# Performance work log

Measured on AMD Instinct MI355X. Metric: run time of the kernel, lower is better.

## Reference

```python
import jax, jax.numpy as jnp
import numpy as np

B, S, H, E, K = 4, 4096, 4096, 64, 2
AUX_W = 0.01


def setup_inputs() -> dict:
    key = jax.random.key(0)
    k1, k2 = jax.random.split(key)
    hidden_states = jax.random.normal(k1, (B, S, H), dtype=jnp.float32)
    W = jax.random.normal(k2, (E, H), dtype=jnp.float32) * 0.02  # router weight [num_experts, hidden_size]
    return {"hidden_states": hidden_states, "W": W}


def reference(hidden_states, W):
    b, s, h = hidden_states.shape
    n = b * s  # tokens
    e, k = W.shape[0], K
    # router logits: [b, s, e] -> [n, e]
    logits = jnp.einsum('bsh,eh->bse', hidden_states, W).reshape(n, e)
    probs = jax.nn.softmax(logits, axis=-1)
    # top-k routing
    routing_weights, selected_experts = jax.lax.top_k(probs, k)  # [n, k]
    routing_weights = routing_weights / jnp.sum(routing_weights, axis=-1, keepdims=True)
    # scatter_add normalized weights back onto expert axis: [n, e]
    rows = jnp.arange(n)[:, None]
    router_prob_per_expert = jnp.zeros((n, e), dtype=probs.dtype).at[rows, selected_experts].add(routing_weights)
    aux_loss = jnp.mean(jnp.sum(router_prob_per_expert, axis=0) * jnp.mean(router_prob_per_expert, axis=0)) * e * AUX_W
    # expert mask via one-hot: [n, k, e]
    dispatch_mask = jax.nn.one_hot(selected_experts, e, dtype=hidden_states.dtype)
    combine_weights = routing_weights.reshape(b, s, k, 1)
    return (dispatch_mask, combine_weights, aux_loss)
```

## Files before the change

kernel.cpp:

```cpp
#include <hip/hip_runtime.h>
#include <cstdint>

#define N_TOK 16384
#define HID   4096
#define NEXP  64
#define AUXW  0.01f
#define TOKB  32
#define KC    64
#define NCH   (HID/KC)
#define IMG_CHUNK 24576

typedef __attribute__((ext_vector_type(4))) _Float16 f16x4;
typedef __attribute__((ext_vector_type(8))) _Float16 f16x8;
typedef __attribute__((ext_vector_type(4))) float f32x4;

typedef const __attribute__((address_space(1))) void gvoid_t;
typedef __attribute__((address_space(3))) void lvoid_t;

__device__ __forceinline__ void async_cp16(const void* g, void* l) {
  __builtin_amdgcn_global_load_lds((gvoid_t*)g, (lvoid_t*)l, 16, 0, 0);
}

__device__ __forceinline__ void split3_f4(float4 p, f16x4& H, f16x4& M, f16x4& L) {
  float f[4] = {p.x, p.y, p.z, p.w};
#pragma unroll
  for (int j = 0; j < 4; ++j) {
    _Float16 h = (_Float16)f[j];
    float r1 = f[j] - (float)h;
    _Float16 m = (_Float16)r1;
    float r2 = r1 - (float)m;
    H[j] = h; M[j] = m; L[j] = (_Float16)r2;
  }
}

__global__ void presplit_w(const float* __restrict__ Wg, char* __restrict__ img) {
  int id = blockIdx.x * 256 + threadIdx.x;
  int row = id >> 9;
  int rem = id & 511;
  int chunk = rem >> 3;
  int g = rem & 7;
  const float* src = Wg + (size_t)row * HID + chunk * KC + g * 8;
  float4 p0 = *(const float4*)src;
  float4 p1 = *(const float4*)(src + 4);
  f16x4 h0, m0, l0, h1, m1, l1;
  split3_f4(p0, h0, m0, l0);
  split3_f4(p1, h1, m1, l1);
  char* base = img + (size_t)chunk * IMG_CHUNK + row * 128 + ((g ^ (row & 7)) << 4);
  *(f16x4*)(base)         = h0;  *(f16x4*)(base + 8)     = h1;
  *(f16x4*)(base + 8192)  = m0;  *(f16x4*)(base + 8200)  = m1;
  *(f16x4*)(base + 16384) = l0;  *(f16x4*)(base + 16392) = l1;
}

__global__ __launch_bounds__(256, 2) void router_main(
    const float* __restrict__ hs, const char* __restrict__ wimg,
    float* __restrict__ out, float* __restrict__ Sacc) {
  __shared__ __align__(16) char smem[61440];
  char* Abuf = smem;
  char* Wb0 = smem + 12288;
  char* Wb1 = smem + 36864;

  const int tid = threadIdx.x;
  const int tb = blockIdx.x * TOKB;
  const int lane = tid & 63;
  const int wv = tid >> 6;
  const int eg = wv & 1, kg = wv >> 1;
  const int l15 = lane & 15, l4 = lane >> 4;

  const int srow = tid >> 3, sg = tid & 7;
  const float* hsp = hs + (size_t)(tb + srow) * HID + sg * 8;
  const int aslot = srow * 128 + ((sg ^ (srow & 7)) << 4);
  const char* wsrc = wimg + tid * 16;

  int aoff[2], boff[2];
#pragma unroll
  for (int tg = 0; tg < 2; ++tg) {
    int r = tg * 16 + l15;
    aoff[tg] = r * 128 + (((kg * 4 + l4) ^ (r & 7)) << 4);
  }
#pragma unroll
  for (int bg = 0; bg < 2; ++bg) {
    int r = eg * 32 + bg * 16 + l15;
    boff[bg] = r * 128 + (((kg * 4 + l4) ^ (r & 7)) << 4);
  }

  f32x4 acc[2][2] = {};
  float4 rA0, rA1, rB0, rB1;

  auto loadhs = [&](int c, float4& x0, float4& x1) {
    x0 = *(const float4*)(hsp + (size_t)c * KC);
    x1 = *(const float4*)(hsp + (size_t)c * KC + 4);
  };
  auto stageW = [&](int c, char* dst) {
#pragma unroll
    for (int it = 0; it < 6; ++it)
      async_cp16(wsrc + (size_t)c * IMG_CHUNK + it * 4096, dst + it * 4096 + tid * 16);
  };
  auto writeA = [&](float4 x0, float4 x1) {
    f16x4 h0, m0, l0, h1, m1, l1;
    split3_f4(x0, h0, m0, l0);
    split3_f4(x1, h1, m1, l1);
    f16x8 H, M, L;
#pragma unroll
    for (int j = 0; j < 4; ++j) {
      H[j] = h0[j]; H[j + 4] = h1[j];
      M[j] = m0[j]; M[j + 4] = m1[j];
      L[j] = l0[j]; L[j + 4] = l1[j];
    }
    *(f16x8*)(Abuf + aslot)        = H;
    *(f16x8*)(Abuf + 4096 + aslot) = M;
    *(f16x8*)(Abuf + 8192 + aslot) = L;
  };
  auto compute = [&](const char* W) {
    f16x8 aH[2], aM[2], aL[2], bH[2], bM[2], bL[2];
#pragma unroll
    for (int t = 0; t < 2; ++t) {
      aH[t] = *(const f16x8*)(Abuf + aoff[t]);
      aM[t] = *(const f16x8*)(Abuf + 4096 + aoff[t]);
      aL[t] = *(const f16x8*)(Abuf + 8192 + aoff[t]);
    }
#pragma unroll
    for (int b = 0; b < 2; ++b) {
      bH[b] = *(const f16x8*)(W + boff[b]);
      bM[b] = *(const f16x8*)(W + 8192 + boff[b]);
      bL[b] = *(const f16x8*)(W + 16384 + boff[b]);
    }
#pragma unroll
    for (int t = 0; t < 2; ++t)
#pragma unroll
      for (int b = 0; b < 2; ++b) {
        f32x4 a = acc[t][b];
        a = __builtin_amdgcn_mfma_f32_16x16x32_f16(aH[t], bH[b], a, 0, 0, 0);
        a = __builtin_amdgcn_mfma_f32_16x16x32_f16(aH[t], bM[b], a, 0, 0, 0);
        a = __builtin_amdgcn_mfma_f32_16x16x32_f16(aM[t], bH[b], a, 0, 0, 0);
        a = __builtin_amdgcn_mfma_f32_16x16x32_f16(aH[t], bL[b], a, 0, 0, 0);
        a = __builtin_amdgcn_mfma_f32_16x16x32_f16(aL[t], bH[b], a, 0, 0, 0);
        a = __builtin_amdgcn_mfma_f32_16x16x32_f16(aM[t], bM[b], a, 0, 0, 0);
        acc[t][b] = a;
      }
  };

  loadhs(0, rA0, rA1);
  stageW(0, Wb0);
  writeA(rA0, rA1);
  loadhs(1, rA0, rA1);
  __syncthreads();

  for (int c = 0; c < NCH - 1; ++c) {
    stageW(c + 1, (c & 1) ? Wb0 : Wb1);
    int cn = (c + 2 < NCH) ? c + 2 : NCH - 1;
    loadhs(cn, rB0, rB1);
    compute((c & 1) ? Wb1 : Wb0);
    asm volatile("s_waitcnt lgkmcnt(0)\n\ts_barrier" ::: "memory");
    writeA(rA0, rA1);
    rA0 = rB0; rA1 = rB1;
    __syncthreads();
  }
  compute((NCH - 1) & 1 ? Wb1 : Wb0);

  float* red   = (float*)(smem + 12288);
  float* lg    = (float*)(smem + 20480);
  float* S_lds = (float*)(smem + 29824);
  int*   e1a   = (int*)(smem + 30080);
  int*   e2a   = (int*)(smem + 30208);

  if (kg == 1) {
#pragma unroll
    for (int t = 0; t < 2; ++t)
#pragma unroll
      for (int b = 0; b < 2; ++b)
#pragma unroll
        for (int r = 0; r < 4; ++r)
          red[(t * 16 + l4 * 4 + r) * 64 + eg * 32 + b * 16 + l15] = acc[t][b][r];
  }
  if (tid < 64) S_lds[tid] = 0.f;
  __syncthreads();
  if (kg == 0) {
#pragma unroll
    for (int t = 0; t < 2; ++t)
#pragma unroll
      for (int b = 0; b < 2; ++b)
#pragma unroll
        for (int r = 0; r < 4; ++r) {
          int tok = t * 16 + l4 * 4 + r, ex = eg * 32 + b * 16 + l15;
          lg[tok * 73 + ex] = acc[t][b][r] + red[tok * 64 + ex];
        }
  }
  __syncthreads();

  if (tid < TOKB) {
    const float* row = lg + tid * 73;
    float m1 = -1e30f, m2 = -1e30f;
    int i1 = 0, i2 = 0;
    for (int e = 0; e < NEXP; ++e) {
      float v = row[e];
      if (v > m1)      { m2 = m1; i2 = i1; m1 = v; i1 = e; }
      else if (v > m2) { m2 = v;  i2 = e; }
    }
    float qq = expf(m2 - m1);
    float w1 = 1.f / (1.f + qq);
    float w2 = qq * w1;
    float* comb = out + (size_t)N_TOK * 2 * NEXP;
    comb[(size_t)(tb + tid) * 2]     = w1;
    comb[(size_t)(tb + tid) * 2 + 1] = w2;
    e1a[tid] = i1; e2a[tid] = i2;
    atomicAdd(&S_lds[i1], w1);
    atomicAdd(&S_lds[i2], w2);
  }
  __syncthreads();
  if (tid < 64) {
    float s = S_lds[tid];
    if (s != 0.f) atomicAdd(&Sacc[tid], s);
  }

#pragma unroll
  for (int it = 0; it < 4; ++it) {
    int f = it * 256 + tid;
    int tok = f >> 5, rem = f & 31, sl = rem >> 4, g = rem & 15;
    int sel = sl ? e2a[tok] : e1a[tok];
    int base = g << 2;
    float4 v;
    v.x = (sel == base)     ? 1.f : 0.f;
    v.y = (sel == base + 1) ? 1.f : 0.f;
    v.z = (sel == base + 2) ? 1.f : 0.f;
    v.w = (sel == base + 3) ? 1.f : 0.f;
    *(float4*)(out + ((size_t)(tb + tok) * 2 + sl) * 64 + base) = v;
  }
}

__global__ void aux_k(const float* __restrict__ S, float* __restrict__ out) {
  float v = S[threadIdx.x];
  float s = v * v;
#pragma unroll
  for (int off = 32; off > 0; off >>= 1) s += __shfl_down(s, off);
  if (threadIdx.x == 0)
    out[(size_t)N_TOK * 2 * NEXP + (size_t)N_TOK * 2] = s * (AUXW / (float)N_TOK);
}

extern "C" void kernel_launch(void* const* d_in, const int* in_sizes, int n_in,
                              void* d_out, int out_size, void* d_ws, size_t ws_size,
                              hipStream_t stream) {
  const float* hs = (const float*)d_in[0];
  const float* Wg = (const float*)d_in[1];
  float* out = (float*)d_out;
  float* S = (float*)d_ws;
  char* img = (char*)d_ws + 256;
  hipMemsetAsync(d_ws, 0, 256, stream);
  hipLaunchKernelGGL(presplit_w, dim3(128), dim3(256), 0, stream, Wg, img);
  hipLaunchKernelGGL(router_main, dim3(N_TOK / TOKB), dim3(256), 0, stream,
                     hs, img, out, S);
  hipLaunchKernelGGL(aux_k, dim3(1), dim3(64), 0, stream, S, out);
}
```

Baseline: 391.2 us.

## Load activations straight to registers and retile router GEMM to 64-token blocks

```diff
diff --git a/kernel.cpp b/kernel.cpp
--- a/kernel.cpp
+++ b/kernel.cpp
@@ -5,10 +5,6 @@
 #define HID   4096
 #define NEXP  64
 #define AUXW  0.01f
-#define TOKB  32
-#define KC    64
-#define NCH   (HID/KC)
-#define IMG_CHUNK 24576
 
 typedef __attribute__((ext_vector_type(4))) _Float16 f16x4;
 typedef __attribute__((ext_vector_type(8))) _Float16 f16x8;
@@ -21,12 +17,11 @@
   __builtin_amdgcn_global_load_lds((gvoid_t*)g, (lvoid_t*)l, 16, 0, 0);
 }
 
-__device__ __forceinline__ void split3_f4(float4 p, f16x4& H, f16x4& M, f16x4& L) {
-  float f[4] = {p.x, p.y, p.z, p.w};
+__device__ __forceinline__ void split3_f4(f32x4 p, f16x4& H, f16x4& M, f16x4& L) {
 #pragma unroll
   for (int j = 0; j < 4; ++j) {
-    _Float16 h = (_Float16)f[j];
-    float r1 = f[j] - (float)h;
+    _Float16 h = (_Float16)p[j];
+    float r1 = p[j] - (float)h;
     _Float16 m = (_Float16)r1;
     float r2 = r1 - (float)m;
     H[j] = h; M[j] = m; L[j] = (_Float16)r2;
@@ -35,159 +30,142 @@
 
 __global__ void presplit_w(const float* __restrict__ Wg, char* __restrict__ img) {
   int id = blockIdx.x * 256 + threadIdx.x;
-  int row = id >> 9;
-  int rem = id & 511;
-  int chunk = rem >> 3;
-  int g = rem & 7;
-  const float* src = Wg + (size_t)row * HID + chunk * KC + g * 8;
-  float4 p0 = *(const float4*)src;
-  float4 p1 = *(const float4*)(src + 4);
+  int r  = id >> 9;
+  int gc = (id >> 2) & 127;
+  int gq = id & 3;
+  const float* src = Wg + (size_t)r * HID + gc * 32 + gq * 8;
+  f32x4 p0 = *(const f32x4*)src;
+  f32x4 p1 = *(const f32x4*)(src + 4);
   f16x4 h0, m0, l0, h1, m1, l1;
   split3_f4(p0, h0, m0, l0);
   split3_f4(p1, h1, m1, l1);
-  char* base = img + (size_t)chunk * IMG_CHUNK + row * 128 + ((g ^ (row & 7)) << 4);
-  *(f16x4*)(base)         = h0;  *(f16x4*)(base + 8)     = h1;
-  *(f16x4*)(base + 8192)  = m0;  *(f16x4*)(base + 8200)  = m1;
-  *(f16x4*)(base + 16384) = l0;  *(f16x4*)(base + 16392) = l1;
-}
-
-__global__ __launch_bounds__(256, 2) void router_main(
+  int step = gc & 63, kg = gc >> 6;
+  char* base = img + (size_t)step * 24576 + kg * 12288 + r * 64 + ((gq ^ (r & 3)) << 4);
+  *(f16x4*)(base)            = h0;  *(f16x4*)(base + 8)        = h1;
+  *(f16x4*)(base + 4096)     = m0;  *(f16x4*)(base + 4096 + 8) = m1;
+  *(f16x4*)(base + 8192)     = l0;  *(f16x4*)(base + 8192 + 8) = l1;
+}
+
+__global__ __launch_bounds__(512) void router_main(
     const float* __restrict__ hs, const char* __restrict__ wimg,
     float* __restrict__ out, float* __restrict__ Sacc) {
-  __shared__ __align__(16) char smem[61440];
-  char* Abuf = smem;
-  char* Wb0 = smem + 12288;
-  char* Wb1 = smem + 36864;
-
+  __shared__ __align__(16) char smem[49152];
   const int tid = threadIdx.x;
-  const int tb = blockIdx.x * TOKB;
-  const int lane = tid & 63;
-  const int wv = tid >> 6;
-  const int eg = wv & 1, kg = wv >> 1;
+  const int lane = tid & 63, wv = tid >> 6;
+  const int tg = wv & 3, kg = wv >> 2;
   const int l15 = lane & 15, l4 = lane >> 4;
-
-  const int srow = tid >> 3, sg = tid & 7;
-  const float* hsp = hs + (size_t)(tb + srow) * HID + sg * 8;
-  const int aslot = srow * 128 + ((sg ^ (srow & 7)) << 4);
-  const char* wsrc = wimg + tid * 16;
-
-  int aoff[2], boff[2];
-#pragma unroll
-  for (int tg = 0; tg < 2; ++tg) {
-    int r = tg * 16 + l15;
-    aoff[tg] = r * 128 + (((kg * 4 + l4) ^ (r & 7)) << 4);
-  }
-#pragma unroll
-  for (int bg = 0; bg < 2; ++bg) {
-    int r = eg * 32 + bg * 16 + l15;
-    boff[bg] = r * 128 + (((kg * 4 + l4) ^ (r & 7)) << 4);
-  }
-
-  f32x4 acc[2][2] = {};
-  float4 rA0, rA1, rB0, rB1;
-
-  auto loadhs = [&](int c, float4& x0, float4& x1) {
-    x0 = *(const float4*)(hsp + (size_t)c * KC);
-    x1 = *(const float4*)(hsp + (size_t)c * KC + 4);
-  };
-  auto stageW = [&](int c, char* dst) {
-#pragma unroll
-    for (int it = 0; it < 6; ++it)
-      async_cp16(wsrc + (size_t)c * IMG_CHUNK + it * 4096, dst + it * 4096 + tid * 16);
-  };
-  auto writeA = [&](float4 x0, float4 x1) {
+  const int tb = blockIdx.x * 64;
+
+  const float* ap = hs + (size_t)(tb + tg * 16 + l15) * HID + kg * 2048 + l4 * 8;
+  const char* wsp = wimg + (size_t)tid * 16;
+
+  int boff[4];
+#pragma unroll
+  for (int eg = 0; eg < 4; ++eg) {
+    int r = eg * 16 + l15;
+    boff[eg] = kg * 12288 + r * 64 + ((l4 ^ (r & 3)) << 4);
+  }
+
+  f32x4 acc[4];
+#pragma unroll
+  for (int eg = 0; eg < 4; ++eg) acc[eg] = (f32x4){0.f, 0.f, 0.f, 0.f};
+
+  auto stage = [&](int c) {
+    char* dst = smem + (c & 1) * 24576;
+#pragma unroll
+    for (int it = 0; it < 3; ++it)
+      async_cp16(wsp + (size_t)c * 24576 + it * 8192, dst + tid * 16 + it * 8192);
+  };
+  auto loadA = [&](int c, f32x4& x, f32x4& y) {
+    const f32x4* p = (const f32x4*)(ap + c * 32);
+    x = __builtin_nontemporal_load(p);
+    y = __builtin_nontemporal_load(p + 1);
+  };
+  auto mk8 = [](f16x4 a, f16x4 b) {
+    f16x8 r;
+#pragma unroll
+    for (int j = 0; j < 4; ++j) { r[j] = a[j]; r[j + 4] = b[j]; }
+    return r;
+  };
+
+  f16x8 aH, aM, aL;
+  auto split_in = [&](f32x4 x, f32x4 y) {
     f16x4 h0, m0, l0, h1, m1, l1;
-    split3_f4(x0, h0, m0, l0);
-    split3_f4(x1, h1, m1, l1);
-    f16x8 H, M, L;
-#pragma unroll
-    for (int j = 0; j < 4; ++j) {
-      H[j] = h0[j]; H[j + 4] = h1[j];
-      M[j] = m0[j]; M[j + 4] = m1[j];
-      L[j] = l0[j]; L[j + 4] = l1[j];
+    split3_f4(x, h0, m0, l0);
+    split3_f4(y, h1, m1, l1);
+    aH = mk8(h0, h1); aM = mk8(m0, m1); aL = mk8(l0, l1);
+  };
+  auto compute = [&](int c) {
+    const char* buf = smem + (c & 1) * 24576;
+#pragma unroll
+    for (int eg = 0; eg < 4; ++eg) {
+      f16x8 bH = *(const f16x8*)(buf + boff[eg]);
+      f16x8 bM = *(const f16x8*)(buf + 4096 + boff[eg]);
+      f16x8 bL = *(const f16x8*)(buf + 8192 + boff[eg]);
+      f32x4 a = acc[eg];
+      a = __builtin_amdgcn_mfma_f32_16x16x32_f16(aH, bH, a, 0, 0, 0);
+      a = __builtin_amdgcn_mfma_f32_16x16x32_f16(aH, bM, a, 0, 0, 0);
+      a = __builtin_amdgcn_mfma_f32_16x16x32_f16(aM, bH, a, 0, 0, 0);
+      a = __builtin_amdgcn_mfma_f32_16x16x32_f16(aH, bL, a, 0, 0, 0);
+      a = __builtin_amdgcn_mfma_f32_16x16x32_f16(aL, bH, a, 0, 0, 0);
+      a = __builtin_amdgcn_mfma_f32_16x16x32_f16(aM, bM, a, 0, 0, 0);
+      acc[eg] = a;
     }
-    *(f16x8*)(Abuf + aslot)        = H;
-    *(f16x8*)(Abuf + 4096 + aslot) = M;
-    *(f16x8*)(Abuf + 8192 + aslot) = L;
-  };
-  auto compute = [&](const char* W) {
-    f16x8 aH[2], aM[2], aL[2], bH[2], bM[2], bL[2];
-#pragma unroll
-    for (int t = 0; t < 2; ++t) {
-      aH[t] = *(const f16x8*)(Abuf + aoff[t]);
-      aM[t] = *(const f16x8*)(Abuf + 4096 + aoff[t]);
-      aL[t] = *(const f16x8*)(Abuf + 8192 + aoff[t]);
-    }
-#pragma unroll
-    for (int b = 0; b < 2; ++b) {
-      bH[b] = *(const f16x8*)(W + boff[b]);
-      bM[b] = *(const f16x8*)(W + 8192 + boff[b]);
-      bL[b] = *(const f16x8*)(W + 16384 + boff[b]);
-    }
-#pragma unroll
-    for (int t = 0; t < 2; ++t)
-#pragma unroll
-      for (int b = 0; b < 2; ++b) {
-        f32x4 a = acc[t][b];
-        a = __builtin_amdgcn_mfma_f32_16x16x32_f16(aH[t], bH[b], a, 0, 0, 0);
-        a = __builtin_amdgcn_mfma_f32_16x16x32_f16(aH[t], bM[b], a, 0, 0, 0);
-        a = __builtin_amdgcn_mfma_f32_16x16x32_f16(aM[t], bH[b], a, 0, 0, 0);
-        a = __builtin_amdgcn_mfma_f32_16x16x32_f16(aH[t], bL[b], a, 0, 0, 0);
-        a = __builtin_amdgcn_mfma_f32_16x16x32_f16(aL[t], bH[b], a, 0, 0, 0);
-        a = __builtin_amdgcn_mfma_f32_16x16x32_f16(aM[t], bM[b], a, 0, 0, 0);
-        acc[t][b] = a;
+  };
+
+  f32x4 a1x, a1y, a2x, a2y, a3x, a3y;
+  stage(0); loadA(0, a1x, a1y); loadA(1, a2x, a2y);
+  stage(1); loadA(2, a3x, a3y);
+  asm volatile("s_waitcnt vmcnt(9)\n\ts_barrier" ::: "memory");
+
+  for (int c = 0; c < 61; ++c) {
+    split_in(a1x, a1y);
+    compute(c);
+    asm volatile("s_waitcnt vmcnt(2)\n\ts_barrier" ::: "memory");
+    stage(c + 2);
+    a1x = a2x; a1y = a2y; a2x = a3x; a2y = a3y;
+    loadA(c + 3, a3x, a3y);
+  }
+  split_in(a1x, a1y);
+  compute(61);
+  asm volatile("s_waitcnt vmcnt(2)\n\ts_barrier" ::: "memory");
+  stage(63);
+  a1x = a2x; a1y = a2y; a2x = a3x; a2y = a3y;
+  split_in(a1x, a1y);
+  compute(62);
+  asm volatile("s_waitcnt vmcnt(0)\n\ts_barrier" ::: "memory");
+  a1x = a2x; a1y = a2y;
+  split_in(a1x, a1y);
+  compute(63);
+  __syncthreads();
+
+  float* red   = (float*)smem;
+  float* lg    = (float*)(smem + 16384);
+  float* S_lds = (float*)(smem + 35072);
+  int*   e1a   = (int*)(smem + 35328);
+  int*   e2a   = (int*)(smem + 35584);
+
+  if (kg == 1) {
+#pragma unroll
+    for (int eg = 0; eg < 4; ++eg)
+#pragma unroll
+      for (int r = 0; r < 4; ++r)
+        red[(tg * 16 + l4 * 4 + r) * 64 + eg * 16 + l15] = acc[eg][r];
+  }
+  if (tid < 64) S_lds[tid] = 0.f;
+  __syncthreads();
+  if (kg == 0) {
+#pragma unroll
+    for (int eg = 0; eg < 4; ++eg)
+#pragma unroll
+      for (int r = 0; r < 4; ++r) {
+        int t = tg * 16 + l4 * 4 + r, e = eg * 16 + l15;
+        lg[t * 73 + e] = acc[eg][r] + red[t * 64 + e];
       }
-  };
-
-  loadhs(0, rA0, rA1);
-  stageW(0, Wb0);
-  writeA(rA0, rA1);
-  loadhs(1, rA0, rA1);
-  __syncthreads();
-
-  for (int c = 0; c < NCH - 1; ++c) {
-    stageW(c + 1, (c & 1) ? Wb0 : Wb1);
-    int cn = (c + 2 < NCH) ? c + 2 : NCH - 1;
-    loadhs(cn, rB0, rB1);
-    compute((c & 1) ? Wb1 : Wb0);
-    asm volatile("s_waitcnt lgkmcnt(0)\n\ts_barrier" ::: "memory");
-    writeA(rA0, rA1);
-    rA0 = rB0; rA1 = rB1;
-    __syncthreads();
-  }
-  compute((NCH - 1) & 1 ? Wb1 : Wb0);
-
-  float* red   = (float*)(smem + 12288);
-  float* lg    = (float*)(smem + 20480);
-  float* S_lds = (float*)(smem + 29824);
-  int*   e1a   = (int*)(smem + 30080);
-  int*   e2a   = (int*)(smem + 30208);
-
-  if (kg == 1) {
-#pragma unroll
-    for (int t = 0; t < 2; ++t)
-#pragma unroll
-      for (int b = 0; b < 2; ++b)
-#pragma unroll
-        for (int r = 0; r < 4; ++r)
-          red[(t * 16 + l4 * 4 + r) * 64 + eg * 32 + b * 16 + l15] = acc[t][b][r];
-  }
-  if (tid < 64) S_lds[tid] = 0.f;
-  __syncthreads();
-  if (kg == 0) {
-#pragma unroll
-    for (int t = 0; t < 2; ++t)
-#pragma unroll
-      for (int b = 0; b < 2; ++b)
-#pragma unroll
-        for (int r = 0; r < 4; ++r) {
-          int tok = t * 16 + l4 * 4 + r, ex = eg * 32 + b * 16 + l15;
-          lg[tok * 73 + ex] = acc[t][b][r] + red[tok * 64 + ex];
-        }
-  }
-  __syncthreads();
-
-  if (tid < TOKB) {
+  }
+  __syncthreads();
+
+  if (tid < 64) {
     const float* row = lg + tid * 73;
     float m1 = -1e30f, m2 = -1e30f;
     int i1 = 0, i2 = 0;
@@ -214,7 +192,7 @@
 
 #pragma unroll
   for (int it = 0; it < 4; ++it) {
-    int f = it * 256 + tid;
+    int f = it * 512 + tid;
     int tok = f >> 5, rem = f & 31, sl = rem >> 4, g = rem & 15;
     int sel = sl ? e2a[tok] : e1a[tok];
     int base = g << 2;
@@ -246,7 +224,7 @@
   char* img = (char*)d_ws + 256;
   hipMemsetAsync(d_ws, 0, 256, stream);
   hipLaunchKernelGGL(presplit_w, dim3(128), dim3(256), 0, stream, Wg, img);
-  hipLaunchKernelGGL(router_main, dim3(N_TOK / TOKB), dim3(256), 0, stream,
+  hipLaunchKernelGGL(router_main, dim3(N_TOK / 64), dim3(512), 0, stream,
                      hs, img, out, S);
   hipLaunchKernelGGL(aux_k, dim3(1), dim3(64), 0, stream, S, out);
 }
```

Result: slower. 413.7 us (+5.7%).
